# Kernel tuning notes

Measured on AMD Instinct MI355X. Metric: run time of the kernel, lower is better.

## Reference

```python
import jax, jax.numpy as jnp
import numpy as np

WINDOW = 11
CHANNEL = 3
SIGMA = 1.5


def _gaussian_kernel():
    coords = jnp.arange(WINDOW, dtype=jnp.float32) - (WINDOW - 1) / 2.0
    g = jnp.exp(-(coords ** 2) / (2.0 * SIGMA ** 2))
    g = g / g.sum()
    k2d = g[:, None] * g[None, :]                      # (k, k)
    # depthwise kernel, OIHW with feature_group_count=C -> (C, 1, k, k)
    return jnp.tile(k2d[None, None], (CHANNEL, 1, 1, 1))


def _dwconv(x, kernel):
    pad = WINDOW // 2
    return jax.lax.conv_general_dilated(
        x, kernel, window_strides=(1, 1),
        padding=((pad, pad), (pad, pad)),
        dimension_numbers=("NCHW", "OIHW", "NCHW"),
        feature_group_count=CHANNEL)


def setup_inputs() -> dict:
    key = jax.random.key(0)
    k1, k2 = jax.random.split(key)
    B, C, H, W = 32, 3, 512, 512
    denoised = jax.random.uniform(k1, (B, C, H, W), dtype=jnp.float32)
    clean = jax.random.uniform(k2, (B, C, H, W), dtype=jnp.float32)
    return {"denoised": denoised, "clean": clean}


def reference(denoised, clean):
    kernel = _gaussian_kernel()
    img1 = jnp.clip(denoised, 0.0, 1.0)
    img2 = jnp.clip(clean, 0.0, 1.0)

    mu1 = _dwconv(img1, kernel)
    mu2 = _dwconv(img2, kernel)
    mu1_sq = mu1 * mu1
    mu2_sq = mu2 * mu2
    mu1_mu2 = mu1 * mu2
    sigma1_sq = _dwconv(img1 * img1, kernel) - mu1_sq
    sigma2_sq = _dwconv(img2 * img2, kernel) - mu2_sq
    sigma12 = _dwconv(img1 * img2, kernel) - mu1_mu2

    C1 = 0.01 ** 2
    C2 = 0.03 ** 2
    ssim_map = ((2.0 * mu1_mu2 + C1) * (2.0 * sigma12 + C2)) / (
        (mu1_sq + mu2_sq + C1) * (sigma1_sq + sigma2_sq + C2))
    return 1.0 - ssim_map.mean()
```

## Files before the change

kernel.cpp:

```cpp
#include <hip/hip_runtime.h>

#define IMG 512
#define OUT_R 16
#define OUT_C 64
#define HALO 5
#define IN_R 26
#define IN_C 74
#define CPAD 80
#define NVTILE 5
#define VS 88
#define NT 256
#define NSLOTS 64

typedef _Float16 f16x8 __attribute__((ext_vector_type(8)));
typedef float    f32x4 __attribute__((ext_vector_type(4)));

static constexpr float GWf[11] = {
    0.00102838f, 0.00759876f, 0.03600077f, 0.10936053f, 0.21300556f,
    0.26601170f, 0.21300556f, 0.10936053f, 0.03600077f, 0.00759876f,
    0.00102838f };

struct WTab { alignas(16) _Float16 v[4][16][8]; };
static constexpr WTab make_wtab() {
    WTab t{};
    for (int g = 0; g < 4; ++g)
        for (int j = 0; j < 16; ++j)
            for (int b = 0; b < 8; ++b) {
                const int d = 8 * g + b - j;
                t.v[g][j][b] = (d >= 0 && d <= 10) ? (_Float16)GWf[d]
                                                   : (_Float16)0.f;
            }
    return t;
}
__device__ constexpr WTab WTAB = make_wtab();

union SMem {
    _Float16 ch[4][CPAD][32];
    struct { _Float16 vb[4][OUT_R][VS]; float red[8]; } s;
};
static_assert(sizeof(SMem) == 4 * CPAD * 32 * 2, "smem size");

__device__ __forceinline__ void prep_task(int task, int c0, int y0,
                                          size_t pbase,
                                          const float* __restrict__ den,
                                          const float* __restrict__ cln,
                                          SMem* sm) {
    const int c = task % CPAD;
    const int g = task / CPAD;
    const int gc = c0 - HALO + c;
    const bool colok = ((unsigned)gc < IMG) && (c < IN_C);
    union { f16x8 v8[4]; _Float16 h[32]; } st;
    const int r0 = g * 8;
#pragma unroll
    for (int rr = 0; rr < 8; ++rr) {
        const int R  = r0 + rr;
        const int gr = y0 - HALO + R;
        float x = 0.f, y = 0.f;
        if (colok && ((unsigned)gr < IMG) && (R < IN_R)) {
            const size_t idx = pbase + (size_t)gr * IMG + gc;
            x = den[idx]; y = cln[idx];
        }
        x = fminf(fmaxf(x, 0.f), 1.f);
        y = fminf(fmaxf(y, 0.f), 1.f);
        st.h[rr]      = (_Float16)x;
        st.h[8 + rr]  = (_Float16)y;
        st.h[16 + rr] = (_Float16)fmaf(x, x, y * y);
        st.h[24 + rr] = (_Float16)(x * y);
    }
    const int slot = g ^ ((c >> 1) & 3);
#pragma unroll
    for (int ch = 0; ch < 4; ++ch)
        *reinterpret_cast<f16x8*>(&sm->ch[ch][c][slot * 8]) = st.v8[ch];
}

__global__ __launch_bounds__(NT, 8)
void ssim_mfma(const float* __restrict__ den, const float* __restrict__ cln,
               double* __restrict__ slots) {
    __shared__ SMem sm;

    const int t    = threadIdx.x;
    const int lane = t & 63;
    const int w    = t >> 6;
    const int fj   = lane & 15;
    const int fg   = lane >> 4;

    const int bid = blockIdx.x;
    int vid = bid;
    if ((gridDim.x & 7) == 0) {
        const int chunk = gridDim.x >> 3;
        vid = (bid & 7) * chunk + (bid >> 3);
    }
    const int rs    = vid & 31;
    const int cs    = (vid >> 5) & 7;
    const int plane = vid >> 8;
    const int c0 = cs * OUT_C;
    const int y0 = rs * OUT_R;
    const size_t pbase = (size_t)plane * (IMG * IMG);

    const f16x8 wf = *reinterpret_cast<const f16x8*>(WTAB.v[fg][fj]);

    prep_task(t, c0, y0, pbase, den, cln, &sm);
    if (t < 4 * CPAD - NT)
        prep_task(NT + t, c0, y0, pbase, den, cln, &sm);
    __syncthreads();

    const f32x4 zero4 = {0.f, 0.f, 0.f, 0.f};
    f32x4 acc[NVTILE];
#pragma unroll
    for (int n = 0; n < NVTILE; ++n) {
        const int tau  = NVTILE * w + n;
        const int tile = tau >> 2;
        const int ch   = tau & 3;
        const int colp = tile * 16 + fj;
        const f16x8 bf = *reinterpret_cast<const f16x8*>(
            &sm.ch[ch][colp][(fg ^ ((colp >> 1) & 3)) * 8]);
        acc[n] = __builtin_amdgcn_mfma_f32_16x16x32_f16(wf, bf, zero4, 0, 0, 0);
    }
    __syncthreads();
#pragma unroll
    for (int n = 0; n < NVTILE; ++n) {
        const int tau  = NVTILE * w + n;
        const int tile = tau >> 2;
        const int ch   = tau & 3;
#pragma unroll
        for (int b = 0; b < 4; ++b)
            sm.s.vb[ch][4 * fg + b][tile * 16 + fj] = (_Float16)acc[n][b];
    }
    __syncthreads();

    float sacc = 0.f;
    {
        const int m = w;
        f32x4 d[4];
#pragma unroll
        for (int ch = 0; ch < 4; ++ch) {
            const f16x8 af = *reinterpret_cast<const f16x8*>(
                &sm.s.vb[ch][fj][m * 16 + 8 * fg]);
            d[ch] = __builtin_amdgcn_mfma_f32_16x16x32_f16(af, wf, zero4, 0, 0, 0);
        }
#pragma unroll
        for (int b = 0; b < 4; ++b) {
            const float C1 = 1e-4f, C2 = 9e-4f;
            const float mu1 = d[0][b], mu2 = d[1][b];
            const float qb  = d[2][b], pb  = d[3][b];
            const float mu1s = mu1 * mu1, mu2s = mu2 * mu2, mu12 = mu1 * mu2;
            const float ssum = qb - mu1s - mu2s;
            const float s12  = pb - mu12;
            const float num  = fmaf(2.f, mu12, C1) * fmaf(2.f, s12, C2);
            const float dnm  = (mu1s + mu2s + C1) * (ssum + C2);
            sacc = fmaf(num, __builtin_amdgcn_rcpf(dnm), sacc);
        }
    }

#pragma unroll
    for (int off = 32; off > 0; off >>= 1)
        sacc += __shfl_down(sacc, off, 64);
    if (lane == 0) sm.s.red[w] = sacc;
    __syncthreads();
    if (t == 0) {
        const float s = sm.s.red[0] + sm.s.red[1] + sm.s.red[2] + sm.s.red[3];
        atomicAdd(&slots[(size_t)(bid & (NSLOTS - 1)) * 8], (double)s);
    }
}

__global__ void ssim_finalize(const double* __restrict__ slots,
                              float* __restrict__ out, double inv_n) {
    double s = 0.0;
    for (int i = 0; i < NSLOTS; ++i) s += slots[i * 8];
    out[0] = 1.0f - (float)(s * inv_n);
}

extern "C" void kernel_launch(void* const* d_in, const int* in_sizes, int n_in,
                              void* d_out, int out_size, void* d_ws,
                              size_t ws_size, hipStream_t stream) {
    const float* den = (const float*)d_in[0];
    const float* cln = (const float*)d_in[1];
    float* out = (float*)d_out;
    double* slots = (double*)d_ws;

    hipMemsetAsync(d_ws, 0, NSLOTS * 64, stream);

    const int n = in_sizes[0];
    const int planes = n / (IMG * IMG);
    dim3 grid(planes * (IMG / OUT_R) * (IMG / OUT_C));
    ssim_mfma<<<grid, NT, 0, stream>>>(den, cln, slots);
    ssim_finalize<<<1, 1, 0, stream>>>(slots, out, 1.0 / (double)n);
}
```

Before: 273.9 us.

## Stream tall row strips through a rolling halo buffer with prefetch

Each block now processes a 128-row strip in 16-row chunks instead of one 16-row tile. The fp16 input rows sit in a circular shared-memory buffer: each iteration loads only the 16 new rows, prefetching them into registers while the vertical MFMA pass runs. This cuts the halo re-reads from about 26/16 of the input to about 1.1x and overlaps global loads with compute. In exchange the grid shrinks by 8x, launch bounds drop to 5 waves, and indexing is more complex because the vertical weight table is shifted to match the ring alignment.

Result: slower. 283.8 us (+3.6%).

```diff
diff --git a/kernel.cpp b/kernel.cpp
--- a/kernel.cpp
+++ b/kernel.cpp
@@ -1,10 +1,11 @@
 #include <hip/hip_runtime.h>
 
 #define IMG 512
-#define OUT_R 16
 #define OUT_C 64
+#define STRIP_R 128
+#define CHUNK 16
+#define NITER (STRIP_R / CHUNK)
 #define HALO 5
-#define IN_R 26
 #define IN_C 74
 #define CPAD 80
 #define NVTILE 5
@@ -13,6 +14,7 @@
 #define NSLOTS 64
 
 typedef _Float16 f16x8 __attribute__((ext_vector_type(8)));
+typedef _Float16 f16x4 __attribute__((ext_vector_type(4)));
 typedef float    f32x4 __attribute__((ext_vector_type(4)));
 
 static constexpr float GWf[11] = {
@@ -21,59 +23,64 @@
     0.00102838f };
 
 struct WTab { alignas(16) _Float16 v[4][16][8]; };
-static constexpr WTab make_wtab() {
+static constexpr WTab make_wtab(int off) {
     WTab t{};
     for (int g = 0; g < 4; ++g)
         for (int j = 0; j < 16; ++j)
             for (int b = 0; b < 8; ++b) {
-                const int d = 8 * g + b - j;
+                const int d = 8 * g + b - j - off;
                 t.v[g][j][b] = (d >= 0 && d <= 10) ? (_Float16)GWf[d]
                                                    : (_Float16)0.f;
             }
     return t;
 }
-__device__ constexpr WTab WTAB = make_wtab();
-
-union SMem {
+__device__ constexpr WTab WV = make_wtab(3);
+__device__ constexpr WTab WH = make_wtab(0);
+
+struct SMem {
     _Float16 ch[4][CPAD][32];
-    struct { _Float16 vb[4][OUT_R][VS]; float red[8]; } s;
+    _Float16 vb[4][CHUNK][VS];
+    float red[4];
 };
-static_assert(sizeof(SMem) == 4 * CPAD * 32 * 2, "smem size");
-
-__device__ __forceinline__ void prep_task(int task, int c0, int y0,
-                                          size_t pbase,
-                                          const float* __restrict__ den,
-                                          const float* __restrict__ cln,
-                                          SMem* sm) {
-    const int c = task % CPAD;
-    const int g = task / CPAD;
+
+__device__ __forceinline__ void load4(int c, int gr0, int c0, size_t pbase,
+                                      const float* __restrict__ den,
+                                      const float* __restrict__ cln,
+                                      float xs[4], float ys[4]) {
     const int gc = c0 - HALO + c;
     const bool colok = ((unsigned)gc < IMG) && (c < IN_C);
-    union { f16x8 v8[4]; _Float16 h[32]; } st;
-    const int r0 = g * 8;
-#pragma unroll
-    for (int rr = 0; rr < 8; ++rr) {
-        const int R  = r0 + rr;
-        const int gr = y0 - HALO + R;
+#pragma unroll
+    for (int rr = 0; rr < 4; ++rr) {
+        const int gr = gr0 + rr;
         float x = 0.f, y = 0.f;
-        if (colok && ((unsigned)gr < IMG) && (R < IN_R)) {
+        if (colok && ((unsigned)gr < IMG)) {
             const size_t idx = pbase + (size_t)gr * IMG + gc;
             x = den[idx]; y = cln[idx];
         }
-        x = fminf(fmaxf(x, 0.f), 1.f);
-        y = fminf(fmaxf(y, 0.f), 1.f);
+        xs[rr] = x; ys[rr] = y;
+    }
+}
+
+__device__ __forceinline__ void store4(int c, int gr0, const float xs[4],
+                                       const float ys[4], SMem* sm) {
+    union { f16x4 v[4]; _Float16 h[16]; } st;
+#pragma unroll
+    for (int rr = 0; rr < 4; ++rr) {
+        const float x = fminf(fmaxf(xs[rr], 0.f), 1.f);
+        const float y = fminf(fmaxf(ys[rr], 0.f), 1.f);
         st.h[rr]      = (_Float16)x;
-        st.h[8 + rr]  = (_Float16)y;
-        st.h[16 + rr] = (_Float16)fmaf(x, x, y * y);
-        st.h[24 + rr] = (_Float16)(x * y);
-    }
-    const int slot = g ^ ((c >> 1) & 3);
+        st.h[4 + rr]  = (_Float16)y;
+        st.h[8 + rr]  = (_Float16)fmaf(x, x, y * y);
+        st.h[12 + rr] = (_Float16)(x * y);
+    }
+    const int s    = (((gr0 + 512) >> 3) & 3) ^ ((c >> 1) & 3);
+    const int half = (gr0 >> 2) & 1;
 #pragma unroll
     for (int ch = 0; ch < 4; ++ch)
-        *reinterpret_cast<f16x8*>(&sm->ch[ch][c][slot * 8]) = st.v8[ch];
-}
-
-__global__ __launch_bounds__(NT, 8)
+        *reinterpret_cast<f16x4*>(&sm->ch[ch][c][s * 8 + half * 4]) = st.v[ch];
+}
+
+__global__ __launch_bounds__(NT, 5)
 void ssim_mfma(const float* __restrict__ den, const float* __restrict__ cln,
                double* __restrict__ slots) {
     __shared__ SMem sm;
@@ -86,79 +93,112 @@
 
     const int bid = blockIdx.x;
     int vid = bid;
-    if ((gridDim.x & 7) == 0) {
+    {
         const int chunk = gridDim.x >> 3;
         vid = (bid & 7) * chunk + (bid >> 3);
     }
-    const int rs    = vid & 31;
-    const int cs    = (vid >> 5) & 7;
-    const int plane = vid >> 8;
+    const int rs    = vid & 3;
+    const int cs    = (vid >> 2) & 7;
+    const int plane = vid >> 5;
     const int c0 = cs * OUT_C;
-    const int y0 = rs * OUT_R;
+    const int y0 = rs * STRIP_R;
     const size_t pbase = (size_t)plane * (IMG * IMG);
 
-    const f16x8 wf = *reinterpret_cast<const f16x8*>(WTAB.v[fg][fj]);
-
-    prep_task(t, c0, y0, pbase, den, cln, &sm);
-    if (t < 4 * CPAD - NT)
-        prep_task(NT + t, c0, y0, pbase, den, cln, &sm);
+    const f16x8 wv = *reinterpret_cast<const f16x8*>(WV.v[fg][fj]);
+    const f16x8 wh = *reinterpret_cast<const f16x8*>(WH.v[fg][fj]);
+    const f32x4 zero4 = {0.f, 0.f, 0.f, 0.f};
+
+#pragma unroll
+    for (int base = 0; base < 640; base += NT) {
+        const int task = base + t;
+        if (task < 640) {
+            const int c  = task % CPAD;
+            const int q  = task / CPAD;
+            const int g0 = y0 - 8 + 4 * q;
+            float xs[4], ys[4];
+            load4(c, g0, c0, pbase, den, cln, xs, ys);
+            store4(c, g0, xs, ys, &sm);
+        }
+    }
     __syncthreads();
 
-    const f32x4 zero4 = {0.f, 0.f, 0.f, 0.f};
-    f32x4 acc[NVTILE];
-#pragma unroll
-    for (int n = 0; n < NVTILE; ++n) {
-        const int tau  = NVTILE * w + n;
-        const int tile = tau >> 2;
-        const int ch   = tau & 3;
-        const int colp = tile * 16 + fj;
-        const f16x8 bf = *reinterpret_cast<const f16x8*>(
-            &sm.ch[ch][colp][(fg ^ ((colp >> 1) & 3)) * 8]);
-        acc[n] = __builtin_amdgcn_mfma_f32_16x16x32_f16(wf, bf, zero4, 0, 0, 0);
-    }
-    __syncthreads();
-#pragma unroll
-    for (int n = 0; n < NVTILE; ++n) {
-        const int tau  = NVTILE * w + n;
-        const int tile = tau >> 2;
-        const int ch   = tau & 3;
-#pragma unroll
-        for (int b = 0; b < 4; ++b)
-            sm.s.vb[ch][4 * fg + b][tile * 16 + fj] = (_Float16)acc[n][b];
-    }
-    __syncthreads();
-
     float sacc = 0.f;
-    {
-        const int m = w;
-        f32x4 d[4];
-#pragma unroll
-        for (int ch = 0; ch < 4; ++ch) {
-            const f16x8 af = *reinterpret_cast<const f16x8*>(
-                &sm.s.vb[ch][fj][m * 16 + 8 * fg]);
-            d[ch] = __builtin_amdgcn_mfma_f32_16x16x32_f16(af, wf, zero4, 0, 0, 0);
-        }
-#pragma unroll
-        for (int b = 0; b < 4; ++b) {
-            const float C1 = 1e-4f, C2 = 9e-4f;
-            const float mu1 = d[0][b], mu2 = d[1][b];
-            const float qb  = d[2][b], pb  = d[3][b];
-            const float mu1s = mu1 * mu1, mu2s = mu2 * mu2, mu12 = mu1 * mu2;
-            const float ssum = qb - mu1s - mu2s;
-            const float s12  = pb - mu12;
-            const float num  = fmaf(2.f, mu12, C1) * fmaf(2.f, s12, C2);
-            const float dnm  = (mu1s + mu2s + C1) * (ssum + C2);
-            sacc = fmaf(num, __builtin_amdgcn_rcpf(dnm), sacc);
+    for (int it = 0; it < NITER; ++it) {
+        const int yo = y0 + CHUNK * it;
+        const bool pf = (it < NITER - 1);
+
+        const int c_0 = t % CPAD, q_0 = t / CPAD;
+        const int g0_ = yo + 24 + 4 * q_0;
+        const int c_1 = (NT + t) % CPAD, q_1 = (NT + t) / CPAD;
+        const int g1_ = yo + 24 + 4 * q_1;
+        float px0[4], py0[4], px1[4], py1[4];
+        if (pf)           load4(c_0, g0_, c0, pbase, den, cln, px0, py0);
+        if (pf && t < 64) load4(c_1, g1_, c0, pbase, den, cln, px1, py1);
+
+        const int ph = (((yo - 8) + 512) >> 3) & 3;
+        f32x4 acc[NVTILE];
+#pragma unroll
+        for (int n = 0; n < NVTILE; ++n) {
+            const int tau  = NVTILE * w + n;
+            const int tile = tau >> 2;
+            const int ch   = tau & 3;
+            const int colp = tile * 16 + fj;
+            const int s    = ((ph + fg) & 3) ^ ((colp >> 1) & 3);
+            const f16x8 bf = *reinterpret_cast<const f16x8*>(
+                &sm.ch[ch][colp][s * 8]);
+            acc[n] = __builtin_amdgcn_mfma_f32_16x16x32_f16(wv, bf, zero4,
+                                                            0, 0, 0);
+        }
+        __syncthreads();
+
+        if (pf) {
+            store4(c_0, g0_, px0, py0, &sm);
+            if (t < 64) store4(c_1, g1_, px1, py1, &sm);
+        }
+#pragma unroll
+        for (int n = 0; n < NVTILE; ++n) {
+            const int tau  = NVTILE * w + n;
+            const int tile = tau >> 2;
+            const int ch   = tau & 3;
+#pragma unroll
+            for (int b = 0; b < 4; ++b)
+                sm.vb[ch][4 * fg + b][tile * 16 + fj] = (_Float16)acc[n][b];
+        }
+        __syncthreads();
+
+        {
+            const int m = w;
+            f32x4 d[4];
+#pragma unroll
+            for (int ch = 0; ch < 4; ++ch) {
+                const f16x8 af = *reinterpret_cast<const f16x8*>(
+                    &sm.vb[ch][fj][m * 16 + 8 * fg]);
+                d[ch] = __builtin_amdgcn_mfma_f32_16x16x32_f16(af, wh, zero4,
+                                                               0, 0, 0);
+            }
+#pragma unroll
+            for (int b = 0; b < 4; ++b) {
+                const float C1 = 1e-4f, C2 = 9e-4f;
+                const float mu1 = d[0][b], mu2 = d[1][b];
+                const float qb  = d[2][b], pb  = d[3][b];
+                const float mu1s = mu1 * mu1, mu2s = mu2 * mu2,
+                            mu12 = mu1 * mu2;
+                const float ssum = qb - mu1s - mu2s;
+                const float s12  = pb - mu12;
+                const float num = fmaf(2.f, mu12, C1) * fmaf(2.f, s12, C2);
+                const float dnm = (mu1s + mu2s + C1) * (ssum + C2);
+                sacc = fmaf(num, __builtin_amdgcn_rcpf(dnm), sacc);
+            }
         }
     }
 
 #pragma unroll
     for (int off = 32; off > 0; off >>= 1)
         sacc += __shfl_down(sacc, off, 64);
-    if (lane == 0) sm.s.red[w] = sacc;
+    if (lane == 0) sm.red[w] = sacc;
     __syncthreads();
     if (t == 0) {
-        const float s = sm.s.red[0] + sm.s.red[1] + sm.s.red[2] + sm.s.red[3];
+        const float s = sm.red[0] + sm.red[1] + sm.red[2] + sm.red[3];
         atomicAdd(&slots[(size_t)(bid & (NSLOTS - 1)) * 8], (double)s);
     }
 }
@@ -182,7 +222,7 @@
 
     const int n = in_sizes[0];
     const int planes = n / (IMG * IMG);
-    dim3 grid(planes * (IMG / OUT_R) * (IMG / OUT_C));
+    dim3 grid(planes * (IMG / STRIP_R) * (IMG / OUT_C));
     ssim_mfma<<<grid, NT, 0, stream>>>(den, cln, slots);
     ssim_finalize<<<1, 1, 0, stream>>>(slots, out, 1.0 / (double)n);
 }
```

## Load inputs directly into MFMA B-fragments, dropping the shared staging pass

Applied to the files above, without the earlier changes.

Each wave now loads its 16-column by 32-row input tile straight from global memory into registers in the MFMA B-operand layout. It computes the clipped, squared and product channels with packed f16 math and runs the vertical MFMAs immediately, so the shared-memory staging buffer and one barrier are gone. The cost is load imbalance: wave 0 handles a fifth tile alone, which lengthens the critical path. Global loads also become per-lane strided rows rather than the previous column-task pattern, and the squared terms are now formed in f16 rather than fp32, which reduces precision. Launch bounds drop from 8 to 6 waves per SIMD.

After: 306.0 us. 11.7% more time.

```diff
diff --git a/kernel.cpp b/kernel.cpp
--- a/kernel.cpp
+++ b/kernel.cpp
@@ -4,15 +4,13 @@
 #define OUT_R 16
 #define OUT_C 64
 #define HALO 5
-#define IN_R 26
-#define IN_C 74
-#define CPAD 80
 #define NVTILE 5
 #define VS 88
 #define NT 256
 #define NSLOTS 64
 
 typedef _Float16 f16x8 __attribute__((ext_vector_type(8)));
+typedef _Float16 h2    __attribute__((ext_vector_type(2)));
 typedef float    f32x4 __attribute__((ext_vector_type(4)));
 
 static constexpr float GWf[11] = {
@@ -32,48 +30,78 @@
             }
     return t;
 }
-__device__ constexpr WTab WTAB = make_wtab();
+__device__ constexpr WTab WT = make_wtab();
 
-union SMem {
-    _Float16 ch[4][CPAD][32];
-    struct { _Float16 vb[4][OUT_R][VS]; float red[8]; } s;
+struct SMem {
+    _Float16 vb[4][OUT_R][VS];
+    float red[4];
 };
-static_assert(sizeof(SMem) == 4 * CPAD * 32 * 2, "smem size");
 
-__device__ __forceinline__ void prep_task(int task, int c0, int y0,
-                                          size_t pbase,
-                                          const float* __restrict__ den,
-                                          const float* __restrict__ cln,
-                                          SMem* sm) {
-    const int c = task % CPAD;
-    const int g = task / CPAD;
-    const int gc = c0 - HALO + c;
-    const bool colok = ((unsigned)gc < IMG) && (c < IN_C);
-    union { f16x8 v8[4]; _Float16 h[32]; } st;
-    const int r0 = g * 8;
-#pragma unroll
-    for (int rr = 0; rr < 8; ++rr) {
-        const int R  = r0 + rr;
-        const int gr = y0 - HALO + R;
-        float x = 0.f, y = 0.f;
-        if (colok && ((unsigned)gr < IMG) && (R < IN_R)) {
-            const size_t idx = pbase + (size_t)gr * IMG + gc;
-            x = den[idx]; y = cln[idx];
-        }
-        x = fminf(fmaxf(x, 0.f), 1.f);
-        y = fminf(fmaxf(y, 0.f), 1.f);
-        st.h[rr]      = (_Float16)x;
-        st.h[8 + rr]  = (_Float16)y;
-        st.h[16 + rr] = (_Float16)fmaf(x, x, y * y);
-        st.h[24 + rr] = (_Float16)(x * y);
-    }
-    const int slot = g ^ ((c >> 1) & 3);
-#pragma unroll
-    for (int ch = 0; ch < 4; ++ch)
-        *reinterpret_cast<f16x8*>(&sm->ch[ch][c][slot * 8]) = st.v8[ch];
+__device__ __forceinline__ h2 cvt_pk(float a, float b) {
+#if __has_builtin(__builtin_amdgcn_cvt_pkrtz)
+    auto r = __builtin_amdgcn_cvt_pkrtz(a, b);
+    union { decltype(r) i; h2 o; } u; u.i = r;
+    return u.o;
+#else
+    h2 r; r[0] = (_Float16)a; r[1] = (_Float16)b; return r;
+#endif
 }
 
-__global__ __launch_bounds__(NT, 8)
+__device__ __forceinline__ void vert_tile(
+    int tl, int c0, int y0, size_t pbase,
+    const float* __restrict__ den, const float* __restrict__ cln,
+    int fj, int fg, f16x8 wf, SMem* sm)
+{
+    const int gc = c0 - HALO + tl * 16 + fj;
+    const bool colok = (unsigned)gc < IMG;
+    const int rbase = y0 - HALO + 8 * fg;
+
+    float xr[8], yr[8];
+#pragma unroll
+    for (int b = 0; b < 8; ++b) {
+        const int gr = rbase + b;
+        const bool ok = colok && ((unsigned)gr < IMG) && (8 * fg + b < 26);
+        float xv = 0.f, yv = 0.f;
+        if (ok) {
+            const size_t idx = pbase + (size_t)gr * IMG + gc;
+            xv = den[idx]; yv = cln[idx];
+        }
+        xr[b] = xv; yr[b] = yv;
+    }
+
+    union { f16x8 v; h2 p[4]; } fx, fy, fq, fp;
+#pragma unroll
+    for (int bb = 0; bb < 4; ++bb) {
+        const float x0 = fminf(fmaxf(xr[2 * bb], 0.f), 1.f);
+        const float x1 = fminf(fmaxf(xr[2 * bb + 1], 0.f), 1.f);
+        const float ya = fminf(fmaxf(yr[2 * bb], 0.f), 1.f);
+        const float yb = fminf(fmaxf(yr[2 * bb + 1], 0.f), 1.f);
+        const h2 xh = cvt_pk(x0, x1);
+        const h2 yh = cvt_pk(ya, yb);
+        fx.p[bb] = xh;
+        fy.p[bb] = yh;
+        fq.p[bb] = xh * xh + yh * yh;
+        fp.p[bb] = xh * yh;
+    }
+
+    const f32x4 zero4 = {0.f, 0.f, 0.f, 0.f};
+    const f32x4 a0 = __builtin_amdgcn_mfma_f32_16x16x32_f16(wf, fx.v, zero4, 0, 0, 0);
+    const f32x4 a1 = __builtin_amdgcn_mfma_f32_16x16x32_f16(wf, fy.v, zero4, 0, 0, 0);
+    const f32x4 a2 = __builtin_amdgcn_mfma_f32_16x16x32_f16(wf, fq.v, zero4, 0, 0, 0);
+    const f32x4 a3 = __builtin_amdgcn_mfma_f32_16x16x32_f16(wf, fp.v, zero4, 0, 0, 0);
+
+    const int cc = tl * 16 + fj;
+#pragma unroll
+    for (int b = 0; b < 4; ++b) {
+        const int r = 4 * fg + b;
+        sm->vb[0][r][cc] = (_Float16)a0[b];
+        sm->vb[1][r][cc] = (_Float16)a1[b];
+        sm->vb[2][r][cc] = (_Float16)a2[b];
+        sm->vb[3][r][cc] = (_Float16)a3[b];
+    }
+}
+
+__global__ __launch_bounds__(NT, 6)
 void ssim_mfma(const float* __restrict__ den, const float* __restrict__ cln,
                double* __restrict__ slots) {
     __shared__ SMem sm;
@@ -85,11 +113,9 @@
     const int fg   = lane >> 4;
 
     const int bid = blockIdx.x;
-    int vid = bid;
-    if ((gridDim.x & 7) == 0) {
-        const int chunk = gridDim.x >> 3;
-        vid = (bid & 7) * chunk + (bid >> 3);
-    }
+    const int chunk = gridDim.x >> 3;
+    const int vid = (bid & 7) * chunk + (bid >> 3);
+
     const int rs    = vid & 31;
     const int cs    = (vid >> 5) & 7;
     const int plane = vid >> 8;
@@ -97,45 +123,21 @@
     const int y0 = rs * OUT_R;
     const size_t pbase = (size_t)plane * (IMG * IMG);
 
-    const f16x8 wf = *reinterpret_cast<const f16x8*>(WTAB.v[fg][fj]);
+    const f16x8 wf = *reinterpret_cast<const f16x8*>(WT.v[fg][fj]);
+    const f32x4 zero4 = {0.f, 0.f, 0.f, 0.f};
 
-    prep_task(t, c0, y0, pbase, den, cln, &sm);
-    if (t < 4 * CPAD - NT)
-        prep_task(NT + t, c0, y0, pbase, den, cln, &sm);
-    __syncthreads();
-
-    const f32x4 zero4 = {0.f, 0.f, 0.f, 0.f};
-    f32x4 acc[NVTILE];
-#pragma unroll
-    for (int n = 0; n < NVTILE; ++n) {
-        const int tau  = NVTILE * w + n;
-        const int tile = tau >> 2;
-        const int ch   = tau & 3;
-        const int colp = tile * 16 + fj;
-        const f16x8 bf = *reinterpret_cast<const f16x8*>(
-            &sm.ch[ch][colp][(fg ^ ((colp >> 1) & 3)) * 8]);
-        acc[n] = __builtin_amdgcn_mfma_f32_16x16x32_f16(wf, bf, zero4, 0, 0, 0);
-    }
-    __syncthreads();
-#pragma unroll
-    for (int n = 0; n < NVTILE; ++n) {
-        const int tau  = NVTILE * w + n;
-        const int tile = tau >> 2;
-        const int ch   = tau & 3;
-#pragma unroll
-        for (int b = 0; b < 4; ++b)
-            sm.s.vb[ch][4 * fg + b][tile * 16 + fj] = (_Float16)acc[n][b];
-    }
+    vert_tile(w, c0, y0, pbase, den, cln, fj, fg, wf, &sm);
+    if (w == 0)
+        vert_tile(4, c0, y0, pbase, den, cln, fj, fg, wf, &sm);
     __syncthreads();
 
     float sacc = 0.f;
     {
-        const int m = w;
         f32x4 d[4];
 #pragma unroll
         for (int ch = 0; ch < 4; ++ch) {
             const f16x8 af = *reinterpret_cast<const f16x8*>(
-                &sm.s.vb[ch][fj][m * 16 + 8 * fg]);
+                &sm.vb[ch][fj][w * 16 + 8 * fg]);
             d[ch] = __builtin_amdgcn_mfma_f32_16x16x32_f16(af, wf, zero4, 0, 0, 0);
         }
 #pragma unroll
@@ -146,8 +148,8 @@
             const float mu1s = mu1 * mu1, mu2s = mu2 * mu2, mu12 = mu1 * mu2;
             const float ssum = qb - mu1s - mu2s;
             const float s12  = pb - mu12;
-            const float num  = fmaf(2.f, mu12, C1) * fmaf(2.f, s12, C2);
-            const float dnm  = (mu1s + mu2s + C1) * (ssum + C2);
+            const float num = fmaf(2.f, mu12, C1) * fmaf(2.f, s12, C2);
+            const float dnm = (mu1s + mu2s + C1) * (ssum + C2);
             sacc = fmaf(num, __builtin_amdgcn_rcpf(dnm), sacc);
         }
     }
@@ -155,10 +157,10 @@
 #pragma unroll
     for (int off = 32; off > 0; off >>= 1)
         sacc += __shfl_down(sacc, off, 64);
-    if (lane == 0) sm.s.red[w] = sacc;
+    if (lane == 0) sm.red[w] = sacc;
     __syncthreads();
     if (t == 0) {
-        const float s = sm.s.red[0] + sm.s.red[1] + sm.s.red[2] + sm.s.red[3];
+        const float s = sm.red[0] + sm.red[1] + sm.red[2] + sm.red[3];
         atomicAdd(&slots[(size_t)(bid & (NSLOTS - 1)) * 8], (double)s);
     }
 }
@@ -178,7 +180,7 @@
     float* out = (float*)d_out;
     double* slots = (double*)d_ws;
 
-    hipMemsetAsync(d_ws, 0, NSLOTS * 64, stream);
+    (void)hipMemsetAsync(d_ws, 0, NSLOTS * 64, stream);
 
     const int n = in_sizes[0];
     const int planes = n / (IMG * IMG);
```
